# Kernel tuning notes

Measured on AMD Instinct MI355X. Metric: run time of the kernel, lower is better.

## Reference

```python
import jax, jax.numpy as jnp
import numpy as np

N_NODES = 50000
N_EDGES = 1600000
C = 128
N_LAYERS = 8


def setup_inputs() -> dict:
    key = jax.random.key(0)
    ks = jax.random.split(key, 10)
    s = lambda fan_in: 1.0 / np.sqrt(fan_in)
    return {
        "x": jax.random.normal(ks[0], (N_NODES, C), dtype=jnp.float32),
        "edge_index": jax.random.randint(ks[1], (2, N_EDGES), 0, N_NODES, dtype=jnp.int32),
        "convs_W": jax.random.normal(ks[2], (N_LAYERS, C, C), dtype=jnp.float32) * s(C),
        "convs_b": jax.random.normal(ks[3], (N_LAYERS, C), dtype=jnp.float32) * s(C),
        "fc0_W": jax.random.normal(ks[4], (2 * C, C), dtype=jnp.float32) * s(2 * C),
        "fc0_b": jax.random.normal(ks[5], (C,), dtype=jnp.float32) * s(2 * C),
        "fc1_W": jax.random.normal(ks[6], (C, C), dtype=jnp.float32) * s(C),
        "fc1_b": jax.random.normal(ks[7], (C,), dtype=jnp.float32) * s(C),
        "fc2_W": jax.random.normal(ks[8], (C, 1), dtype=jnp.float32) * s(C),
        "fc2_b": jax.random.normal(ks[9], (1,), dtype=jnp.float32) * s(C),
    }


def reference(x, edge_index, convs_W, convs_b, fc0_W, fc0_b, fc1_W, fc1_b, fc2_W, fc2_b):
    N = x.shape[0]
    row, col = edge_index[0], edge_index[1]

    # GCNConv default: add self-loops, symmetric D^{-1/2}(A+I)D^{-1/2} normalization
    loops = jnp.arange(N, dtype=row.dtype)
    row_sl = jnp.concatenate([row, loops])  # source of message
    col_sl = jnp.concatenate([col, loops])  # target of aggregation
    deg = jax.ops.segment_sum(jnp.ones(row_sl.shape[0], x.dtype), col_sl, num_segments=N)
    dis = jnp.where(deg > 0, jax.lax.rsqrt(deg), 0.0)
    norm = dis[row_sl] * dis[col_sl]  # [E + N]

    def gcn_conv(h, W, b):
        h = h @ W                                  # [N, C]
        msg = h[row_sl] * norm[:, None]            # [E+N, C] gather + scale
        agg = jax.ops.segment_sum(msg, col_sl, num_segments=N)
        return agg + b

    h = jax.nn.relu(gcn_conv(x, convs_W[0], convs_b[0]))
    for i in range(1, convs_W.shape[0]):
        h = jax.nn.relu(gcn_conv(h, convs_W[i], convs_b[i]) + h)

    # edge MLP classifier on cat([h[src], h[dst]])
    e = jnp.concatenate([h[row], h[col]], axis=1)  # [E, 2C]
    e = jax.nn.relu(e @ fc0_W + fc0_b)
    e = jax.nn.relu(e @ fc1_W + fc1_b)
    return e @ fc2_W + fc2_b                       # [E, 1]
```

## Files before the change

### kernel.cpp

```cpp
#include <hip/hip_runtime.h>

#define C 128

typedef __attribute__((ext_vector_type(4))) float float4v;
typedef _Float16 half8v __attribute__((ext_vector_type(8)));
typedef _Float16 half4v __attribute__((ext_vector_type(4)));

__global__ void k_degree(const int* __restrict__ col, int* __restrict__ cnt, int E) {
  int e = blockIdx.x * blockDim.x + threadIdx.x;
  if (e < E) atomicAdd(&cnt[col[e]], 1);
}

__global__ void k_scan_part(const int* __restrict__ cnt, int* __restrict__ part,
                            int N) {
  __shared__ int sb[256];
  int t = threadIdx.x;
  int i = blockIdx.x * 256 + t;
  sb[t] = (i < N) ? cnt[i] : 0;
  __syncthreads();
#pragma unroll
  for (int off = 128; off > 0; off >>= 1) {
    if (t < off) sb[t] += sb[t + off];
    __syncthreads();
  }
  if (t == 0) part[blockIdx.x] = sb[0];
}

__global__ void k_scan_mid(int* __restrict__ part, int P) {
  __shared__ int sb[256];
  int t = threadIdx.x;
  int v = (t < P) ? part[t] : 0;
  sb[t] = v;
  __syncthreads();
#pragma unroll
  for (int off = 1; off < 256; off <<= 1) {
    int u = (t >= off) ? sb[t - off] : 0;
    __syncthreads();
    sb[t] += u;
    __syncthreads();
  }
  if (t < P) part[t] = sb[t] - v;
}

__global__ void k_scan_fin(const int* __restrict__ cnt, const int* __restrict__ part,
                           float* __restrict__ dis, int* __restrict__ indptr,
                           int* __restrict__ cursor, int N) {
  __shared__ int sb[256];
  int t = threadIdx.x;
  int i = blockIdx.x * 256 + t;
  int v = (i < N) ? cnt[i] : 0;
  sb[t] = v;
  __syncthreads();
#pragma unroll
  for (int off = 1; off < 256; off <<= 1) {
    int u = (t >= off) ? sb[t - off] : 0;
    __syncthreads();
    sb[t] += u;
    __syncthreads();
  }
  int run = part[blockIdx.x] + sb[t] - v;
  if (i < N) {
    indptr[i] = run;
    cursor[i] = run;
    dis[i] = rsqrtf((float)(v + 1));
    if (i == N - 1) indptr[N] = run + v;
  }
}

__global__ void k_csrfill(const int* __restrict__ row, const int* __restrict__ col,
                          const float* __restrict__ dis, int* __restrict__ cursor,
                          int2* __restrict__ emeta, int* __restrict__ inv, int E) {
  int e = blockIdx.x * blockDim.x + threadIdx.x;
  if (e >= E) return;
  int r = row[e], c = col[e];
  int pos = atomicAdd(&cursor[c], 1);
  float nrm = dis[r] * dis[c];
  emeta[pos] = make_int2(r, __float_as_int(nrm));
  inv[e] = pos;
}

__global__ void k_colfill(const int* __restrict__ indptr, int* __restrict__ colcsr,
                          int N) {
  int w = (blockIdx.x * 256 + threadIdx.x) >> 6;
  int lane = threadIdx.x & 63;
  if (w >= N) return;
  int s = indptr[w], e = indptr[w + 1];
  for (int i = s + lane; i < e; i += 64) colcsr[i] = w;
}

__global__ void k_cvt(const float* __restrict__ x, _Float16* __restrict__ xh, int n4) {
  int i = blockIdx.x * 256 + threadIdx.x;
  if (i >= n4) return;
  float4 v = ((const float4*)x)[i];
  half4v o = {(_Float16)v.x, (_Float16)v.y, (_Float16)v.z, (_Float16)v.w};
  *(half4v*)(xh + i * 4) = o;
}

__global__ void k_prepwf(const float* __restrict__ W1, _Float16* __restrict__ Wf) {
  int idx = blockIdx.x * 256 + threadIdx.x;
  int e = idx & 7, lane = (idx >> 3) & 63, j = (idx >> 9) & 7, kk = idx >> 12;
  int n = j * 16 + (lane & 15);
  int k = (kk * 4 + (lane >> 4)) * 8 + e;
  Wf[idx] = (_Float16)W1[k * C + n];
}

__global__ void k_prepw2(const float* __restrict__ convs_W,
                         const float* __restrict__ fc0_W,
                         _Float16* __restrict__ Wfh, _Float16* __restrict__ Wfl) {
  int g = blockIdx.x * 256 + threadIdx.x;
  int mat = g >> 14, idx = g & 16383;
  int e = idx & 7, lane = (idx >> 3) & 63, j = (idx >> 9) & 7, kk = idx >> 12;
  int n = j * 16 + (lane & 15);
  int k = (kk * 4 + (lane >> 4)) * 8 + e;
  const float* src = (mat < 8) ? convs_W + ((size_t)mat << 14)
                               : fc0_W + ((size_t)(mat - 8) << 14);
  float v = src[k * C + n];
  _Float16 h = (_Float16)v;
  Wfh[g] = h;
  Wfl[g] = (_Float16)((v - (float)h) * 4096.f);
}

__global__ __launch_bounds__(256)
void k_agg(const _Float16* __restrict__ h, const int* __restrict__ indptr,
           const int2* __restrict__ emeta, const float* __restrict__ dis,
           _Float16* __restrict__ agg, int N) {
  int w = (blockIdx.x * 256 + threadIdx.x) >> 6;
  int lane = threadIdx.x & 63;
  if (w >= N) return;
  int g16 = lane >> 4, c8 = lane & 15;
  int s = indptr[w], e = indptr[w + 1];

  float dv = 0.f;
  half8v hs = {};
  if (lane < 16) {
    dv = dis[w];
    hs = *(const half8v*)(h + (size_t)w * C + lane * 8);
  }

  float acc[8];
#pragma unroll
  for (int j = 0; j < 8; ++j) acc[j] = 0.f;

  int i = s;
  if (i + 32 <= e) {
    long long mm = __builtin_nontemporal_load(
        (const long long*)&emeta[i + (lane & 31)]);
    for (;;) {
      int inext = i + 32;
      bool hn = (inext + 32 <= e);
      long long mmn = 0;
      if (hn)
        mmn = __builtin_nontemporal_load(
            (const long long*)&emeta[inext + (lane & 31)]);
      long long mu[8];
#pragma unroll
      for (int u = 0; u < 8; ++u) mu[u] = __shfl(mm, u * 4 + g16, 64);
      half8v hv[8];
#pragma unroll
      for (int u = 0; u < 8; ++u) {
        int srcn = (int)(mu[u] & 0xffffffffLL);
        hv[u] = *(const half8v*)(h + (size_t)srcn * C + c8 * 8);
      }
#pragma unroll
      for (int u = 0; u < 8; ++u) {
        float nn = __int_as_float((int)(mu[u] >> 32));
#pragma unroll
        for (int j = 0; j < 8; ++j) acc[j] += nn * (float)hv[u][j];
      }
      i = inext;
      if (!hn) break;
      mm = mmn;
    }
  }
  if (i + 16 <= e) {
    long long mc[4];
#pragma unroll
    for (int u = 0; u < 4; ++u)
      mc[u] = __builtin_nontemporal_load(
          (const long long*)&emeta[i + u * 4 + g16]);
    half8v hv[4];
#pragma unroll
    for (int u = 0; u < 4; ++u) {
      int srcn = (int)(mc[u] & 0xffffffffLL);
      hv[u] = *(const half8v*)(h + (size_t)srcn * C + c8 * 8);
    }
#pragma unroll
    for (int u = 0; u < 4; ++u) {
      float nn = __int_as_float((int)(mc[u] >> 32));
#pragma unroll
      for (int j = 0; j < 8; ++j) acc[j] += nn * (float)hv[u][j];
    }
    i += 16;
  }
  for (; i + 4 <= e; i += 4) {
    long long m = __builtin_nontemporal_load((const long long*)&emeta[i + g16]);
    int srcn = (int)(m & 0xffffffffLL);
    half8v hv = *(const half8v*)(h + (size_t)srcn * C + c8 * 8);
    float nn = __int_as_float((int)(m >> 32));
#pragma unroll
    for (int j = 0; j < 8; ++j) acc[j] += nn * (float)hv[j];
  }
  if (i < e) {
    int idx = i + g16;
    int srcn = w;
    float nn = 0.f;
    if (idx < e) {
      long long m = __builtin_nontemporal_load((const long long*)&emeta[idx]);
      srcn = (int)(m & 0xffffffffLL);
      nn = __int_as_float((int)(m >> 32));
    }
    half8v hv = *(const half8v*)(h + (size_t)srcn * C + c8 * 8);
#pragma unroll
    for (int j = 0; j < 8; ++j) acc[j] += nn * (float)hv[j];
  }
#pragma unroll
  for (int j = 0; j < 8; ++j) {
    acc[j] += __shfl_xor(acc[j], 16, 64);
    acc[j] += __shfl_xor(acc[j], 32, 64);
  }
  if (lane < 16) {
    float dv2 = dv * dv;
    half8v o;
#pragma unroll
    for (int j = 0; j < 8; ++j) o[j] = (_Float16)(acc[j] + dv2 * (float)hs[j]);
    *(half8v*)(agg + (size_t)w * C + lane * 8) = o;
  }
}

__global__ __launch_bounds__(256, 4)
void k_gemm_f16(const _Float16* __restrict__ A,
                const _Float16* __restrict__ Wfh, const _Float16* __restrict__ Wfl,
                const float* __restrict__ bias, const _Float16* __restrict__ skip,
                _Float16* __restrict__ out, int M, int relu) {
  int t = threadIdx.x;
  int r0 = blockIdx.x * 64;
  int w = t >> 6, lane = t & 63;
  int m0 = w * 16, lm = lane & 15, lq = lane >> 4;
  int row = r0 + m0 + lm;
  if (row >= M) row = M - 1;
  const _Float16* Ar = A + (size_t)row * C;

  float4v acch[8], accl[8];
#pragma unroll
  for (int j = 0; j < 8; ++j) {
    acch[j] = (float4v){0.f, 0.f, 0.f, 0.f};
    accl[j] = (float4v){0.f, 0.f, 0.f, 0.f};
  }
#pragma unroll
  for (int kk = 0; kk < 4; ++kk) {
    half8v a = *(const half8v*)(Ar + kk * 32 + lq * 8);
#pragma unroll
    for (int j = 0; j < 8; ++j) {
      int fi = ((kk * 8 + j) * 64 + lane) << 3;
      half8v bh = *(const half8v*)(Wfh + fi);
      half8v bl = *(const half8v*)(Wfl + fi);
      acch[j] = __builtin_amdgcn_mfma_f32_16x16x32_f16(a, bh, acch[j], 0, 0, 0);
      accl[j] = __builtin_amdgcn_mfma_f32_16x16x32_f16(a, bl, accl[j], 0, 0, 0);
    }
  }
#pragma unroll
  for (int j = 0; j < 8; ++j) {
    int n = j * 16 + lm;
    float bv = bias ? bias[n] : 0.f;
#pragma unroll
    for (int r = 0; r < 4; ++r) {
      int m = r0 + m0 + lq * 4 + r;
      if (m >= M) continue;
      float v = acch[j][r] + accl[j][r] * (1.f / 4096.f) + bv;
      if (skip) v += (float)skip[(size_t)m * C + n];
      if (relu) v = fmaxf(v, 0.f);
      out[(size_t)m * C + n] = (_Float16)v;
    }
  }
}

__global__ __launch_bounds__(256, 4)
void k_gemm_fc0(const _Float16* __restrict__ A,
                const _Float16* __restrict__ Wfh, const _Float16* __restrict__ Wfl,
                const float* __restrict__ b0,
                _Float16* __restrict__ Pm, _Float16* __restrict__ Qm, int M) {
  int t = threadIdx.x;
  int r0 = blockIdx.x * 64;
  int w = t >> 6, lane = t & 63;
  int m0 = w * 16, lm = lane & 15, lq = lane >> 4;
  int row = r0 + m0 + lm;
  if (row >= M) row = M - 1;
  const _Float16* Ar = A + (size_t)row * C;
  half8v a[4];
#pragma unroll
  for (int kk = 0; kk < 4; ++kk) a[kk] = *(const half8v*)(Ar + kk * 32 + lq * 8);

#pragma unroll
  for (int half = 0; half < 2; ++half) {
    const _Float16* Bh = Wfh + half * (C * C);
    const _Float16* Bl = Wfl + half * (C * C);
    float4v acch[8], accl[8];
#pragma unroll
    for (int j = 0; j < 8; ++j) {
      acch[j] = (float4v){0.f, 0.f, 0.f, 0.f};
      accl[j] = (float4v){0.f, 0.f, 0.f, 0.f};
    }
#pragma unroll
    for (int kk = 0; kk < 4; ++kk) {
#pragma unroll
      for (int j = 0; j < 8; ++j) {
        int fi = ((kk * 8 + j) * 64 + lane) << 3;
        half8v bh = *(const half8v*)(Bh + fi);
        half8v bl = *(const half8v*)(Bl + fi);
        acch[j] = __builtin_amdgcn_mfma_f32_16x16x32_f16(a[kk], bh, acch[j], 0, 0, 0);
        accl[j] = __builtin_amdgcn_mfma_f32_16x16x32_f16(a[kk], bl, accl[j], 0, 0, 0);
      }
    }
    _Float16* outp = half ? Qm : Pm;
#pragma unroll
    for (int j = 0; j < 8; ++j) {
      int n = j * 16 + lm;
      float bv = half ? b0[n] : 0.f;
#pragma unroll
      for (int r = 0; r < 4; ++r) {
        int m = r0 + m0 + lq * 4 + r;
        if (m >= M) continue;
        float v = acch[j][r] + accl[j][r] * (1.f / 4096.f) + bv;
        outp[(size_t)m * C + n] = (_Float16)v;
      }
    }
  }
}

__global__ __launch_bounds__(256, 4)
void k_edge(const _Float16* __restrict__ P, const _Float16* __restrict__ Q,
            const int2* __restrict__ emeta, const int* __restrict__ colcsr,
            const _Float16* __restrict__ Wf,
            const float* __restrict__ b1, const float* __restrict__ w2,
            const float* __restrict__ b2, float* __restrict__ tmpout, int E) {
  __shared__ __align__(16) _Float16 WL[16384];
  int t = threadIdx.x;
#pragma unroll
  for (int it = 0; it < 8; ++it) {
    int off = it * 2048 + t * 8;
    *(half8v*)(WL + off) = *(const half8v*)(Wf + off);
  }

  int w = t >> 6, lane = t & 63;
  int lm = lane & 15, lq = lane >> 4;
  int base = blockIdx.x * 128 + w * 32;

  half8v a[2][4];
#pragma unroll
  for (int tt = 0; tt < 2; ++tt) {
    int p = base + tt * 16 + lm;
    int pc = (p < E) ? p : (E - 1);
    long long ev = __builtin_nontemporal_load((const long long*)&emeta[pc]);
    int rx = (int)(ev & 0xffffffffLL);
    int ry = __builtin_nontemporal_load(&colcsr[pc]);
    const _Float16* Pp = P + (size_t)rx * C + lq * 8;
    const _Float16* Qp = Q + (size_t)ry * C + lq * 8;
#pragma unroll
    for (int kk = 0; kk < 4; ++kk) {
      half8v pa = *(const half8v*)(Pp + kk * 32);
      half8v qa = *(const half8v*)(Qp + kk * 32);
      half8v s = pa + qa;
#pragma unroll
      for (int j = 0; j < 8; ++j)
        s[j] = (s[j] > (_Float16)0.f) ? s[j] : (_Float16)0.f;
      a[tt][kk] = s;
    }
  }
  __syncthreads();

  float4v acc[2][8];
#pragma unroll
  for (int tt = 0; tt < 2; ++tt)
#pragma unroll
    for (int j = 0; j < 8; ++j) acc[tt][j] = (float4v){0.f, 0.f, 0.f, 0.f};

#pragma unroll
  for (int kk = 0; kk < 4; ++kk) {
#pragma unroll
    for (int j = 0; j < 8; ++j) {
      half8v b = *(const half8v*)(WL + (((kk * 8 + j) * 64 + lane) << 3));
#pragma unroll
      for (int tt = 0; tt < 2; ++tt)
        acc[tt][j] = __builtin_amdgcn_mfma_f32_16x16x32_f16(a[tt][kk], b,
                                                            acc[tt][j], 0, 0, 0);
    }
  }

  float b1v[8], w2v[8];
#pragma unroll
  for (int j = 0; j < 8; ++j) {
    int n = j * 16 + lm;
    b1v[j] = b1[n];
    w2v[j] = w2[n];
  }
  float bb = b2[0];
#pragma unroll
  for (int tt = 0; tt < 2; ++tt) {
    float partv[4] = {0.f, 0.f, 0.f, 0.f};
#pragma unroll
    for (int j = 0; j < 8; ++j) {
#pragma unroll
      for (int r = 0; r < 4; ++r) {
        float e2 = fmaxf(acc[tt][j][r] + b1v[j], 0.f);
        partv[r] = fmaf(e2, w2v[j], partv[r]);
      }
    }
#pragma unroll
    for (int off = 1; off < 16; off <<= 1) {
#pragma unroll
      for (int r = 0; r < 4; ++r) partv[r] += __shfl_xor(partv[r], off, 64);
    }
    if (lm == 0) {
#pragma unroll
      for (int r = 0; r < 4; ++r) {
        int pe = base + tt * 16 + lq * 4 + r;
        if (pe < E) __builtin_nontemporal_store(partv[r] + bb, &tmpout[pe]);
      }
    }
  }
}

__global__ void k_perm(const float* __restrict__ tmp, const int* __restrict__ inv,
                       float* __restrict__ out, int E) {
  int e = blockIdx.x * 256 + threadIdx.x;
  if (e < E) {
    int idx = __builtin_nontemporal_load(&inv[e]);
    float v = tmp[idx];
    __builtin_nontemporal_store(v, &out[e]);
  }
}

extern "C" void kernel_launch(void* const* d_in, const int* in_sizes, int n_in,
                              void* d_out, int out_size, void* d_ws, size_t ws_size,
                              hipStream_t stream) {
  const float* x       = (const float*)d_in[0];
  const int*   ei      = (const int*)d_in[1];
  const float* convs_W = (const float*)d_in[2];
  const float* convs_b = (const float*)d_in[3];
  const float* fc0_W   = (const float*)d_in[4];
  const float* fc0_b   = (const float*)d_in[5];
  const float* fc1_W   = (const float*)d_in[6];
  const float* fc1_b   = (const float*)d_in[7];
  const float* fc2_W   = (const float*)d_in[8];
  const float* fc2_b   = (const float*)d_in[9];
  float* out = (float*)d_out;

  const int N = in_sizes[0] / C;
  const int E = in_sizes[1] / 2;
  const int L = in_sizes[2] / (C * C);
  const int* row = ei;
  const int* col = ei + E;
  const int SB = (N + 255) / 256;

  char* wp = (char*)d_ws;
  auto carve = [&](size_t bytes) {
    char* p = wp; wp += (bytes + 255) & ~(size_t)255; return p;
  };
  int*      cnt    = (int*)carve((size_t)N * 4);
  int*      part   = (int*)carve((size_t)SB * 4);
  int*      indptr = (int*)carve((size_t)(N + 1) * 4);
  int*      cursor = (int*)carve((size_t)N * 4);
  float*    dis    = (float*)carve((size_t)N * 4);
  int2*     emeta  = (int2*)carve((size_t)E * 8);
  int*      colcsr = (int*)carve((size_t)E * 4);
  int*      inv    = (int*)carve((size_t)E * 4);
  float*    tmpout = (float*)carve((size_t)E * 4);
  _Float16* Wf     = (_Float16*)carve((size_t)C * C * 2);
  _Float16* Wfh    = (_Float16*)carve((size_t)10 * C * C * 2);
  _Float16* Wfl    = (_Float16*)carve((size_t)10 * C * C * 2);
  _Float16* xh     = (_Float16*)carve((size_t)N * C * 2);
  _Float16* h0     = (_Float16*)carve((size_t)N * C * 2);
  _Float16* h1     = (_Float16*)carve((size_t)N * C * 2);
  _Float16* aggb   = (_Float16*)carve((size_t)N * C * 2);
  _Float16* Pm     = (_Float16*)carve((size_t)N * C * 2);
  _Float16* Qm     = (_Float16*)carve((size_t)N * C * 2);

  hipMemsetAsync(cnt, 0, (size_t)N * 4, stream);
  k_degree<<<(E + 255) / 256, 256, 0, stream>>>(col, cnt, E);
  k_scan_part<<<SB, 256, 0, stream>>>(cnt, part, N);
  k_scan_mid<<<1, 256, 0, stream>>>(part, SB);
  k_scan_fin<<<SB, 256, 0, stream>>>(cnt, part, dis, indptr, cursor, N);
  k_csrfill<<<(E + 255) / 256, 256, 0, stream>>>(row, col, dis, cursor,
                                                 emeta, inv, E);
  k_colfill<<<(N * 64 + 255) / 256, 256, 0, stream>>>(indptr, colcsr, N);
  k_prepwf<<<C * C / 256, 256, 0, stream>>>(fc1_W, Wf);
  k_prepw2<<<10 * C * C / 256, 256, 0, stream>>>(convs_W, fc0_W, Wfh, Wfl);
  k_cvt<<<(N * C / 4 + 255) / 256, 256, 0, stream>>>(x, xh, N * C / 4);

  int aggBlocks  = (N * 64 + 255) / 256;
  int gemmBlocks = (N + 63) / 64;
  const int MSZ = C * C;

  k_agg<<<aggBlocks, 256, 0, stream>>>(xh, indptr, emeta, dis, aggb, N);
  k_gemm_f16<<<gemmBlocks, 256, 0, stream>>>(aggb, Wfh, Wfl, convs_b,
                                             nullptr, h0, N, 1);
  _Float16* hcur = h0; _Float16* hoth = h1;
  for (int l = 1; l < L; ++l) {
    k_agg<<<aggBlocks, 256, 0, stream>>>(hcur, indptr, emeta, dis, aggb, N);
    k_gemm_f16<<<gemmBlocks, 256, 0, stream>>>(aggb, Wfh + (size_t)l * MSZ,
                                               Wfl + (size_t)l * MSZ,
                                               convs_b + (size_t)l * C, hcur,
                                               hoth, N, 1);
    _Float16* tmp = hcur; hcur = hoth; hoth = tmp;
  }
  k_gemm_fc0<<<gemmBlocks, 256, 0, stream>>>(hcur, Wfh + (size_t)8 * MSZ,
                                             Wfl + (size_t)8 * MSZ, fc0_b,
                                             Pm, Qm, N);
  k_edge<<<(E + 127) / 128, 256, 0, stream>>>(Pm, Qm, emeta, colcsr, Wf, fc1_b,
                                              fc2_W, fc2_b, tmpout, E);
  k_perm<<<(E + 255) / 256, 256, 0, stream>>>(tmpout, inv, out, E);
}
```

Before: 1.057 ms.

## Fuse neighbor aggregation into per-layer GCN GEMM via shared-memory tile

Merges the aggregation and GEMM kernels into a single kernel. Each wave now aggregates 16 destination nodes one after another, stages the fp16 results in LDS, then feeds them to the MFMA GEMM. This removes the intermediate aggregation buffer round-trip through global memory and one kernel launch per layer. In exchange, far fewer waves are in flight: one wave per 16 nodes instead of one per node. That reduces the latency hiding available to the irregular neighbor gathers.

```diff
diff --git a/kernel.cpp b/kernel.cpp
--- a/kernel.cpp
+++ b/kernel.cpp
@@ -121,124 +121,126 @@
 }
 
 __global__ __launch_bounds__(256)
-void k_agg(const _Float16* __restrict__ h, const int* __restrict__ indptr,
-           const int2* __restrict__ emeta, const float* __restrict__ dis,
-           _Float16* __restrict__ agg, int N) {
-  int w = (blockIdx.x * 256 + threadIdx.x) >> 6;
-  int lane = threadIdx.x & 63;
-  if (w >= N) return;
-  int g16 = lane >> 4, c8 = lane & 15;
-  int s = indptr[w], e = indptr[w + 1];
-
-  float dv = 0.f;
-  half8v hs = {};
-  if (lane < 16) {
-    dv = dis[w];
-    hs = *(const half8v*)(h + (size_t)w * C + lane * 8);
-  }
-
-  float acc[8];
-#pragma unroll
-  for (int j = 0; j < 8; ++j) acc[j] = 0.f;
-
-  int i = s;
-  if (i + 32 <= e) {
-    long long mm = __builtin_nontemporal_load(
-        (const long long*)&emeta[i + (lane & 31)]);
-    for (;;) {
-      int inext = i + 32;
-      bool hn = (inext + 32 <= e);
-      long long mmn = 0;
-      if (hn)
-        mmn = __builtin_nontemporal_load(
-            (const long long*)&emeta[inext + (lane & 31)]);
-      long long mu[8];
-#pragma unroll
-      for (int u = 0; u < 8; ++u) mu[u] = __shfl(mm, u * 4 + g16, 64);
-      half8v hv[8];
-#pragma unroll
-      for (int u = 0; u < 8; ++u) {
-        int srcn = (int)(mu[u] & 0xffffffffLL);
-        hv[u] = *(const half8v*)(h + (size_t)srcn * C + c8 * 8);
-      }
-#pragma unroll
-      for (int u = 0; u < 8; ++u) {
-        float nn = __int_as_float((int)(mu[u] >> 32));
-#pragma unroll
-        for (int j = 0; j < 8; ++j) acc[j] += nn * (float)hv[u][j];
-      }
-      i = inext;
-      if (!hn) break;
-      mm = mmn;
-    }
-  }
-  if (i + 16 <= e) {
-    long long mc[4];
-#pragma unroll
-    for (int u = 0; u < 4; ++u)
-      mc[u] = __builtin_nontemporal_load(
-          (const long long*)&emeta[i + u * 4 + g16]);
-    half8v hv[4];
-#pragma unroll
-    for (int u = 0; u < 4; ++u) {
-      int srcn = (int)(mc[u] & 0xffffffffLL);
-      hv[u] = *(const half8v*)(h + (size_t)srcn * C + c8 * 8);
-    }
-#pragma unroll
-    for (int u = 0; u < 4; ++u) {
-      float nn = __int_as_float((int)(mc[u] >> 32));
-#pragma unroll
-      for (int j = 0; j < 8; ++j) acc[j] += nn * (float)hv[u][j];
-    }
-    i += 16;
-  }
-  for (; i + 4 <= e; i += 4) {
-    long long m = __builtin_nontemporal_load((const long long*)&emeta[i + g16]);
-    int srcn = (int)(m & 0xffffffffLL);
-    half8v hv = *(const half8v*)(h + (size_t)srcn * C + c8 * 8);
-    float nn = __int_as_float((int)(m >> 32));
-#pragma unroll
-    for (int j = 0; j < 8; ++j) acc[j] += nn * (float)hv[j];
-  }
-  if (i < e) {
-    int idx = i + g16;
-    int srcn = w;
-    float nn = 0.f;
-    if (idx < e) {
-      long long m = __builtin_nontemporal_load((const long long*)&emeta[idx]);
-      srcn = (int)(m & 0xffffffffLL);
-      nn = __int_as_float((int)(m >> 32));
-    }
-    half8v hv = *(const half8v*)(h + (size_t)srcn * C + c8 * 8);
-#pragma unroll
-    for (int j = 0; j < 8; ++j) acc[j] += nn * (float)hv[j];
-  }
-#pragma unroll
-  for (int j = 0; j < 8; ++j) {
-    acc[j] += __shfl_xor(acc[j], 16, 64);
-    acc[j] += __shfl_xor(acc[j], 32, 64);
-  }
-  if (lane < 16) {
-    float dv2 = dv * dv;
-    half8v o;
-#pragma unroll
-    for (int j = 0; j < 8; ++j) o[j] = (_Float16)(acc[j] + dv2 * (float)hs[j]);
-    *(half8v*)(agg + (size_t)w * C + lane * 8) = o;
-  }
-}
-
-__global__ __launch_bounds__(256, 4)
-void k_gemm_f16(const _Float16* __restrict__ A,
+void k_agg_gemm(const _Float16* __restrict__ h, const int* __restrict__ indptr,
+                const int2* __restrict__ emeta, const float* __restrict__ dis,
                 const _Float16* __restrict__ Wfh, const _Float16* __restrict__ Wfl,
                 const float* __restrict__ bias, const _Float16* __restrict__ skip,
-                _Float16* __restrict__ out, int M, int relu) {
+                _Float16* __restrict__ out, int N, int relu) {
+  __shared__ __align__(16) _Float16 AL[4][16][136];
   int t = threadIdx.x;
+  int w = t >> 6, lane = t & 63;
+  int g16 = lane >> 4, c8 = lane & 15;
   int r0 = blockIdx.x * 64;
-  int w = t >> 6, lane = t & 63;
+  int nb = r0 + w * 16;
+
+  for (int i = 0; i < 16; ++i) {
+    int nd = nb + i;
+    float acc[8];
+#pragma unroll
+    for (int j = 0; j < 8; ++j) acc[j] = 0.f;
+    float dv = 0.f;
+    half8v hs = {};
+    if (nd < N) {
+      if (lane < 16) {
+        dv = dis[nd];
+        hs = *(const half8v*)(h + (size_t)nd * C + lane * 8);
+      }
+      int s = indptr[nd], e = indptr[nd + 1];
+      int ii = s;
+      if (ii + 32 <= e) {
+        long long mm = __builtin_nontemporal_load(
+            (const long long*)&emeta[ii + (lane & 31)]);
+        for (;;) {
+          int inext = ii + 32;
+          bool hn = (inext + 32 <= e);
+          long long mmn = 0;
+          if (hn)
+            mmn = __builtin_nontemporal_load(
+                (const long long*)&emeta[inext + (lane & 31)]);
+          long long mu[8];
+#pragma unroll
+          for (int u = 0; u < 8; ++u) mu[u] = __shfl(mm, u * 4 + g16, 64);
+          half8v hv[8];
+#pragma unroll
+          for (int u = 0; u < 8; ++u) {
+            int srcn = (int)(mu[u] & 0xffffffffLL);
+            hv[u] = *(const half8v*)(h + (size_t)srcn * C + c8 * 8);
+          }
+#pragma unroll
+          for (int u = 0; u < 8; ++u) {
+            float nn = __int_as_float((int)(mu[u] >> 32));
+#pragma unroll
+            for (int j = 0; j < 8; ++j) acc[j] += nn * (float)hv[u][j];
+          }
+          ii = inext;
+          if (!hn) break;
+          mm = mmn;
+        }
+      }
+      if (ii + 16 <= e) {
+        long long mc[4];
+#pragma unroll
+        for (int u = 0; u < 4; ++u)
+          mc[u] = __builtin_nontemporal_load(
+              (const long long*)&emeta[ii + u * 4 + g16]);
+        half8v hv[4];
+#pragma unroll
+        for (int u = 0; u < 4; ++u) {
+          int srcn = (int)(mc[u] & 0xffffffffLL);
+          hv[u] = *(const half8v*)(h + (size_t)srcn * C + c8 * 8);
+        }
+#pragma unroll
+        for (int u = 0; u < 4; ++u) {
+          float nn = __int_as_float((int)(mc[u] >> 32));
+#pragma unroll
+          for (int j = 0; j < 8; ++j) acc[j] += nn * (float)hv[u][j];
+        }
+        ii += 16;
+      }
+      for (; ii + 4 <= e; ii += 4) {
+        long long m = __builtin_nontemporal_load(
+            (const long long*)&emeta[ii + g16]);
+        int srcn = (int)(m & 0xffffffffLL);
+        half8v hv = *(const half8v*)(h + (size_t)srcn * C + c8 * 8);
+        float nn = __int_as_float((int)(m >> 32));
+#pragma unroll
+        for (int j = 0; j < 8; ++j) acc[j] += nn * (float)hv[j];
+      }
+      if (ii < e) {
+        int idx = ii + g16;
+        int srcn = nd;
+        float nn = 0.f;
+        if (idx < e) {
+          long long m = __builtin_nontemporal_load(
+              (const long long*)&emeta[idx]);
+          srcn = (int)(m & 0xffffffffLL);
+          nn = __int_as_float((int)(m >> 32));
+        }
+        half8v hv = *(const half8v*)(h + (size_t)srcn * C + c8 * 8);
+#pragma unroll
+        for (int j = 0; j < 8; ++j) acc[j] += nn * (float)hv[j];
+      }
+    }
+#pragma unroll
+    for (int j = 0; j < 8; ++j) {
+      acc[j] += __shfl_xor(acc[j], 16, 64);
+      acc[j] += __shfl_xor(acc[j], 32, 64);
+    }
+    if (lane < 16) {
+      float dv2 = dv * dv;
+      half8v o;
+#pragma unroll
+      for (int j = 0; j < 8; ++j)
+        o[j] = (_Float16)(acc[j] + dv2 * (float)hs[j]);
+      *(half8v*)&AL[w][i][lane * 8] = o;
+    }
+  }
+
   int m0 = w * 16, lm = lane & 15, lq = lane >> 4;
-  int row = r0 + m0 + lm;
-  if (row >= M) row = M - 1;
-  const _Float16* Ar = A + (size_t)row * C;
+  half8v a[4];
+#pragma unroll
+  for (int kk = 0; kk < 4; ++kk)
+    a[kk] = *(const half8v*)&AL[w][lm][kk * 32 + lq * 8];
 
   float4v acch[8], accl[8];
 #pragma unroll
@@ -248,24 +250,23 @@
   }
 #pragma unroll
   for (int kk = 0; kk < 4; ++kk) {
-    half8v a = *(const half8v*)(Ar + kk * 32 + lq * 8);
 #pragma unroll
     for (int j = 0; j < 8; ++j) {
       int fi = ((kk * 8 + j) * 64 + lane) << 3;
       half8v bh = *(const half8v*)(Wfh + fi);
       half8v bl = *(const half8v*)(Wfl + fi);
-      acch[j] = __builtin_amdgcn_mfma_f32_16x16x32_f16(a, bh, acch[j], 0, 0, 0);
-      accl[j] = __builtin_amdgcn_mfma_f32_16x16x32_f16(a, bl, accl[j], 0, 0, 0);
+      acch[j] = __builtin_amdgcn_mfma_f32_16x16x32_f16(a[kk], bh, acch[j], 0, 0, 0);
+      accl[j] = __builtin_amdgcn_mfma_f32_16x16x32_f16(a[kk], bl, accl[j], 0, 0, 0);
     }
   }
 #pragma unroll
   for (int j = 0; j < 8; ++j) {
     int n = j * 16 + lm;
-    float bv = bias ? bias[n] : 0.f;
+    float bv = bias[n];
 #pragma unroll
     for (int r = 0; r < 4; ++r) {
       int m = r0 + m0 + lq * 4 + r;
-      if (m >= M) continue;
+      if (m >= N) continue;
       float v = acch[j][r] + accl[j][r] * (1.f / 4096.f) + bv;
       if (skip) v += (float)skip[(size_t)m * C + n];
       if (relu) v = fmaxf(v, 0.f);
@@ -471,7 +472,6 @@
   _Float16* xh     = (_Float16*)carve((size_t)N * C * 2);
   _Float16* h0     = (_Float16*)carve((size_t)N * C * 2);
   _Float16* h1     = (_Float16*)carve((size_t)N * C * 2);
-  _Float16* aggb   = (_Float16*)carve((size_t)N * C * 2);
   _Float16* Pm     = (_Float16*)carve((size_t)N * C * 2);
   _Float16* Qm     = (_Float16*)carve((size_t)N * C * 2);
 
@@ -487,17 +487,15 @@
   k_prepw2<<<10 * C * C / 256, 256, 0, stream>>>(convs_W, fc0_W, Wfh, Wfl);
   k_cvt<<<(N * C / 4 + 255) / 256, 256, 0, stream>>>(x, xh, N * C / 4);
 
-  int aggBlocks  = (N * 64 + 255) / 256;
   int gemmBlocks = (N + 63) / 64;
   const int MSZ = C * C;
 
-  k_agg<<<aggBlocks, 256, 0, stream>>>(xh, indptr, emeta, dis, aggb, N);
-  k_gemm_f16<<<gemmBlocks, 256, 0, stream>>>(aggb, Wfh, Wfl, convs_b,
-                                             nullptr, h0, N, 1);
+  k_agg_gemm<<<gemmBlocks, 256, 0, stream>>>(xh, indptr, emeta, dis, Wfh, Wfl,
+                                             convs_b, nullptr, h0, N, 1);
   _Float16* hcur = h0; _Float16* hoth = h1;
   for (int l = 1; l < L; ++l) {
-    k_agg<<<aggBlocks, 256, 0, stream>>>(hcur, indptr, emeta, dis, aggb, N);
-    k_gemm_f16<<<gemmBlocks, 256, 0, stream>>>(aggb, Wfh + (size_t)l * MSZ,
+    k_agg_gemm<<<gemmBlocks, 256, 0, stream>>>(hcur, indptr, emeta, dis,
+                                               Wfh + (size_t)l * MSZ,
                                                Wfl + (size_t)l * MSZ,
                                                convs_b + (size_t)l * C, hcur,
                                                hoth, N, 1);
```

New measurement: 1.526 ms. 44.3% more time.

## Run edge MLP in original edge order, dropping colfill and output permutation

Applied to the files above, without the earlier changes.

The edge classifier now reads source and destination indices straight from edge_index and writes results directly to the output in original edge order. This removes the colcsr fill kernel, the inverse-permutation array written by csrfill, the temporary output buffer and the final permutation kernel. The cost is that edge-kernel gathers of P and Q rows lose the destination-sorted locality the CSR order gave for Q, so those gathers become more random.

```diff
diff --git a/kernel.cpp b/kernel.cpp
--- a/kernel.cpp
+++ b/kernel.cpp
@@ -69,23 +69,13 @@
 
 __global__ void k_csrfill(const int* __restrict__ row, const int* __restrict__ col,
                           const float* __restrict__ dis, int* __restrict__ cursor,
-                          int2* __restrict__ emeta, int* __restrict__ inv, int E) {
+                          int2* __restrict__ emeta, int E) {
   int e = blockIdx.x * blockDim.x + threadIdx.x;
   if (e >= E) return;
   int r = row[e], c = col[e];
   int pos = atomicAdd(&cursor[c], 1);
   float nrm = dis[r] * dis[c];
   emeta[pos] = make_int2(r, __float_as_int(nrm));
-  inv[e] = pos;
-}
-
-__global__ void k_colfill(const int* __restrict__ indptr, int* __restrict__ colcsr,
-                          int N) {
-  int w = (blockIdx.x * 256 + threadIdx.x) >> 6;
-  int lane = threadIdx.x & 63;
-  if (w >= N) return;
-  int s = indptr[w], e = indptr[w + 1];
-  for (int i = s + lane; i < e; i += 64) colcsr[i] = w;
 }
 
 __global__ void k_cvt(const float* __restrict__ x, _Float16* __restrict__ xh, int n4) {
@@ -329,10 +319,10 @@
 
 __global__ __launch_bounds__(256, 4)
 void k_edge(const _Float16* __restrict__ P, const _Float16* __restrict__ Q,
-            const int2* __restrict__ emeta, const int* __restrict__ colcsr,
+            const int* __restrict__ row, const int* __restrict__ col,
             const _Float16* __restrict__ Wf,
             const float* __restrict__ b1, const float* __restrict__ w2,
-            const float* __restrict__ b2, float* __restrict__ tmpout, int E) {
+            const float* __restrict__ b2, float* __restrict__ out, int E) {
   __shared__ __align__(16) _Float16 WL[16384];
   int t = threadIdx.x;
 #pragma unroll
@@ -350,9 +340,8 @@
   for (int tt = 0; tt < 2; ++tt) {
     int p = base + tt * 16 + lm;
     int pc = (p < E) ? p : (E - 1);
-    long long ev = __builtin_nontemporal_load((const long long*)&emeta[pc]);
-    int rx = (int)(ev & 0xffffffffLL);
-    int ry = __builtin_nontemporal_load(&colcsr[pc]);
+    int rx = __builtin_nontemporal_load(&row[pc]);
+    int ry = __builtin_nontemporal_load(&col[pc]);
     const _Float16* Pp = P + (size_t)rx * C + lq * 8;
     const _Float16* Qp = Q + (size_t)ry * C + lq * 8;
 #pragma unroll
@@ -414,19 +403,9 @@
 #pragma unroll
       for (int r = 0; r < 4; ++r) {
         int pe = base + tt * 16 + lq * 4 + r;
-        if (pe < E) __builtin_nontemporal_store(partv[r] + bb, &tmpout[pe]);
-      }
-    }
-  }
-}
-
-__global__ void k_perm(const float* __restrict__ tmp, const int* __restrict__ inv,
-                       float* __restrict__ out, int E) {
-  int e = blockIdx.x * 256 + threadIdx.x;
-  if (e < E) {
-    int idx = __builtin_nontemporal_load(&inv[e]);
-    float v = tmp[idx];
-    __builtin_nontemporal_store(v, &out[e]);
+        if (pe < E) __builtin_nontemporal_store(partv[r] + bb, &out[pe]);
+      }
+    }
   }
 }
 
@@ -462,9 +441,6 @@
   int*      cursor = (int*)carve((size_t)N * 4);
   float*    dis    = (float*)carve((size_t)N * 4);
   int2*     emeta  = (int2*)carve((size_t)E * 8);
-  int*      colcsr = (int*)carve((size_t)E * 4);
-  int*      inv    = (int*)carve((size_t)E * 4);
-  float*    tmpout = (float*)carve((size_t)E * 4);
   _Float16* Wf     = (_Float16*)carve((size_t)C * C * 2);
   _Float16* Wfh    = (_Float16*)carve((size_t)10 * C * C * 2);
   _Float16* Wfl    = (_Float16*)carve((size_t)10 * C * C * 2);
@@ -481,8 +457,7 @@
   k_scan_mid<<<1, 256, 0, stream>>>(part, SB);
   k_scan_fin<<<SB, 256, 0, stream>>>(cnt, part, dis, indptr, cursor, N);
   k_csrfill<<<(E + 255) / 256, 256, 0, stream>>>(row, col, dis, cursor,
-                                                 emeta, inv, E);
-  k_colfill<<<(N * 64 + 255) / 256, 256, 0, stream>>>(indptr, colcsr, N);
+                                                 emeta, E);
   k_prepwf<<<C * C / 256, 256, 0, stream>>>(fc1_W, Wf);
   k_prepw2<<<10 * C * C / 256, 256, 0, stream>>>(convs_W, fc0_W, Wfh, Wfl);
   k_cvt<<<(N * C / 4 + 255) / 256, 256, 0, stream>>>(x, xh, N * C / 4);
@@ -506,7 +481,6 @@
   k_gemm_fc0<<<gemmBlocks, 256, 0, stream>>>(hcur, Wfh + (size_t)8 * MSZ,
                                              Wfl + (size_t)8 * MSZ, fc0_b,
                                              Pm, Qm, N);
-  k_edge<<<(E + 127) / 128, 256, 0, stream>>>(Pm, Qm, emeta, colcsr, Wf, fc1_b,
-                                              fc2_W, fc2_b, tmpout, E);
-  k_perm<<<(E + 255) / 256, 256, 0, stream>>>(tmpout, inv, out, E);
-}
+  k_edge<<<(E + 127) / 128, 256, 0, stream>>>(Pm, Qm, row, col, Wf, fc1_b,
+                                              fc2_W, fc2_b, out, E);
+}
```

Measured after the change: 1.073 ms. Within noise of the previous version (+1.4%).
